# Kernel tuning notes

Hardware: AMD Instinct MI355X
Metric: run time of the kernel (lower is better)

Reference implementation:

```python
import jax, jax.numpy as jnp
import numpy as np

N_ITERS = 3  # Set2Set n_iters


def _set2set(feat, gid, B, Wih, Whh, bih, bhh):
    # DGL Set2Set with n_iters=3, n_layers=1: LSTM(input=2D, hidden=D), PyTorch gate order i,f,g,o
    N, D = feat.shape
    q_star = jnp.zeros((B, 2 * D), feat.dtype)
    h = jnp.zeros((B, D), feat.dtype)
    c = jnp.zeros((B, D), feat.dtype)
    bias = bih + bhh
    for _ in range(N_ITERS):
        gates = q_star @ Wih.T + h @ Whh.T + bias  # (B, 4D)
        i, f, g, o = jnp.split(gates, 4, axis=-1)
        i = jax.nn.sigmoid(i); f = jax.nn.sigmoid(f); o = jax.nn.sigmoid(o); g = jnp.tanh(g)
        c = f * c + i * g
        h = o * jnp.tanh(c)  # q = h, shape (B, D)
        e = jnp.sum(feat * h[gid], axis=-1)  # (N,) attention logits
        m = jax.ops.segment_max(e, gid, num_segments=B, indices_are_sorted=True)
        ex = jnp.exp(e - m[gid])
        s = jax.ops.segment_sum(ex, gid, num_segments=B, indices_are_sorted=True)
        alpha = ex / s[gid]  # segment softmax
        readout = jax.ops.segment_sum(feat * alpha[:, None], gid, num_segments=B, indices_are_sorted=True)
        q_star = jnp.concatenate([h, readout], axis=-1)  # (B, 2D)
    return q_star


def setup_inputs() -> dict:
    key = jax.random.key(0)
    ks = jax.random.split(key, 18)
    N, E, D, B, OUT = 100000, 1000000, 64, 64, 1
    s = 1.0 / np.sqrt(D)
    u = lambda k, shp, b: jax.random.uniform(k, shp, jnp.float32, -b, b)
    inp = {
        'feat': jax.random.normal(ks[0], (N, D), jnp.float32),
        'efeat': jax.random.normal(ks[1], (E, D), jnp.float32),
        'edge_dst': jax.random.randint(ks[2], (E,), 0, N, jnp.int32),
        'node_graph': jnp.sort(jax.random.randint(ks[3], (N,), 0, B, jnp.int32)),
        'n_graphs': B,
        'node_Wih': u(ks[4], (4 * D, 2 * D), s), 'node_Whh': u(ks[5], (4 * D, D), s),
        'node_bih': u(ks[6], (4 * D,), s), 'node_bhh': u(ks[7], (4 * D,), s),
        'edge_Wih': u(ks[8], (4 * D, 2 * D), s), 'edge_Whh': u(ks[9], (4 * D, D), s),
        'edge_bih': u(ks[10], (4 * D,), s), 'edge_bhh': u(ks[11], (4 * D,), s),
        'W1': u(ks[12], (32, 4 * D), np.sqrt(6.0 / (4 * D + 32)) * np.sqrt(2.0)),
        'b1': jnp.zeros((32,), jnp.float32),
        'W2': u(ks[13], (16, 32), np.sqrt(6.0 / 48) * np.sqrt(2.0)),
        'b2': jnp.zeros((16,), jnp.float32),
        'W3': u(ks[14], (OUT, 16), np.sqrt(6.0 / (16 + OUT)) * np.sqrt(2.0)),
        'b3': jnp.zeros((OUT,), jnp.float32),
    }
    return inp


def reference(feat, efeat, edge_dst, node_graph, n_graphs,
              node_Wih, node_Whh, node_bih, node_bhh,
              edge_Wih, edge_Whh, edge_bih, edge_bhh,
              W1, b1, W2, b2, W3, b3):
    N = feat.shape[0]
    # mpnn = identity: node_emb = feat, edge_emb = efeat
    node_s2s = _set2set(feat, node_graph, n_graphs, node_Wih, node_Whh, node_bih, node_bhh)
    # graph.update_all(fn.copy_e, fn.mean): scatter-mean of edge features onto dst nodes
    deg = jax.ops.segment_sum(jnp.ones((efeat.shape[0],), feat.dtype), edge_dst, num_segments=N)
    edge_agg = jax.ops.segment_sum(efeat, edge_dst, num_segments=N) / jnp.maximum(deg, 1.0)[:, None]
    edge_s2s = _set2set(edge_agg, node_graph, n_graphs, edge_Wih, edge_Whh, edge_bih, edge_bhh)
    out = jnp.concatenate([node_s2s, edge_s2s], axis=1)  # (B, 4D)
    out = jax.nn.relu(out @ W1.T + b1)
    out = jax.nn.relu(out @ W2.T + b2)
    out = out @ W3.T + b3
    return out
```

## Files before the change

### kernel.cpp

```cpp
#include <hip/hip_runtime.h>
#include <math.h>

#define D 64
#define B 64
#define NPB 128
#define NSLOT 4
#define SCAN_BS 1024

__device__ __forceinline__ unsigned encf(float x) {
  unsigned u = __float_as_uint(x);
  return (u & 0x80000000u) ? ~u : (u | 0x80000000u);
}
__device__ __forceinline__ float decf(unsigned e) {
  return (e & 0x80000000u) ? __uint_as_float(e ^ 0x80000000u) : __uint_as_float(~e);
}
__device__ __forceinline__ float sigm(float x) { return 1.0f / (1.0f + __expf(-x)); }


__global__ void k_deg(const int* __restrict__ edge_dst, int* __restrict__ deg, int E) {
  int i = blockIdx.x * blockDim.x + threadIdx.x;
  if (i < E) atomicAdd(&deg[edge_dst[i]], 1);
}

__global__ void k_scan1(const int* __restrict__ deg, int* __restrict__ row_start,
                        int* __restrict__ blocksum, int N) {
  __shared__ int sm[SCAN_BS];
  int t = threadIdx.x;
  int base = blockIdx.x * SCAN_BS;
  int v = (base + t < N) ? deg[base + t] : 0;
  sm[t] = v;
  __syncthreads();
  for (int ofs = 1; ofs < SCAN_BS; ofs <<= 1) {
    int add = (t >= ofs) ? sm[t - ofs] : 0;
    __syncthreads();
    sm[t] += add;
    __syncthreads();
  }
  if (base + t < N) row_start[base + t] = sm[t] - v;
  if (t == SCAN_BS - 1) blocksum[blockIdx.x] = sm[t];
}

__global__ void k_scan2(int* __restrict__ blocksum, int nb) {
  __shared__ int sm[128];
  int t = threadIdx.x;
  int v = (t < nb) ? blocksum[t] : 0;
  sm[t] = v;
  __syncthreads();
  for (int ofs = 1; ofs < 128; ofs <<= 1) {
    int add = (t >= ofs) ? sm[t - ofs] : 0;
    __syncthreads();
    sm[t] += add;
    __syncthreads();
  }
  if (t < nb) blocksum[t] = sm[t] - v;
}

__global__ void k_scan3(int* __restrict__ row_start, const int* __restrict__ blocksum,
                        int* __restrict__ cursor, int N) {
  int n = blockIdx.x * blockDim.x + threadIdx.x;
  if (n < N) {
    int v = row_start[n] + blocksum[n / SCAN_BS];
    row_start[n] = v;
    cursor[n] = v;
  }
}

__global__ void k_fill(const int* __restrict__ edge_dst, int* __restrict__ cursor,
                       int* __restrict__ csr, int E) {
  int e = blockIdx.x * blockDim.x + threadIdx.x;
  if (e < E) {
    int dst = edge_dst[e];
    int idx = atomicAdd(&cursor[dst], 1);
    csr[idx] = e;
  }
}

__global__ void k_gather(const float* __restrict__ efeat, const int* __restrict__ csr,
                         const int* __restrict__ row_start, const int* __restrict__ deg,
                         float* __restrict__ edge_agg, int N) {
  int grp = (blockIdx.x * blockDim.x + threadIdx.x) >> 4;
  int l16 = threadIdx.x & 15;
  if (grp >= N) return;
  int base = row_start[grp];
  int dg = deg[grp];
  float4 acc = make_float4(0.f, 0.f, 0.f, 0.f);
  for (int i = 0; i < dg; i += 16) {
    int idx[16];
    #pragma unroll
    for (int j = 0; j < 16; ++j) {
      int k = i + j;
      idx[j] = csr[base + (k < dg ? k : dg - 1)];
    }
    #pragma unroll
    for (int j = 0; j < 16; ++j) {
      float4 v = *(const float4*)(efeat + (size_t)idx[j] * D + l16 * 4);
      bool ok = (i + j < dg);
      acc.x += ok ? v.x : 0.0f;
      acc.y += ok ? v.y : 0.0f;
      acc.z += ok ? v.z : 0.0f;
      acc.w += ok ? v.w : 0.0f;
    }
  }
  float inv = 1.0f / fmaxf((float)dg, 1.0f);
  acc.x *= inv; acc.y *= inv; acc.z *= inv; acc.w *= inv;
  *(float4*)(edge_agg + (size_t)grp * D + l16 * 4) = acc;
}


__global__ void k_lstm2(int first, float* __restrict__ h2, float* __restrict__ c2,
                        float* __restrict__ s2, float* __restrict__ r2,
                        unsigned* __restrict__ m2, float* __restrict__ off2,
                        const float* __restrict__ nWih, const float* __restrict__ nWhh,
                        const float* __restrict__ nbih, const float* __restrict__ nbhh,
                        const float* __restrict__ eWih, const float* __restrict__ eWhh,
                        const float* __restrict__ ebih, const float* __restrict__ ebhh) {
  __shared__ float sq[2 * D], sg[4 * D];
  int side = blockIdx.y;
  const float* Wih = side ? eWih : nWih;
  const float* Whh = side ? eWhh : nWhh;
  const float* bih = side ? ebih : nbih;
  const float* bhh = side ? ebhh : nbhh;
  float* h = h2 + side * B * D;
  float* c = c2 + side * B * D;
  float* s_buf = s2 + side * B;
  float* r_buf = r2 + side * B * D;

  int b = blockIdx.x, j = threadIdx.x;
  if (j < D) {
    sq[j] = h[b * D + j];
  } else if (j < 2 * D) {
    sq[j] = first ? 0.0f : (r_buf[b * D + (j - D)] / s_buf[b]);
  }
  __syncthreads();
  float acc = bih[j] + bhh[j];
  const float* wr = Wih + (size_t)j * (2 * D);
  #pragma unroll 8
  for (int k = 0; k < 2 * D; ++k) acc += sq[k] * wr[k];
  const float* wr2 = Whh + (size_t)j * D;
  #pragma unroll 8
  for (int k = 0; k < D; ++k) acc += sq[k] * wr2[k];
  sg[j] = acc;
  __syncthreads();
  if (j < D) {
    float ig = sigm(sg[j]);
    float fg = sigm(sg[D + j]);
    float gg = tanhf(sg[2 * D + j]);
    float og = sigm(sg[3 * D + j]);
    float cn = fg * c[b * D + j] + ig * gg;
    c[b * D + j] = cn;
    h[b * D + j] = og * tanhf(cn);
    r_buf[b * D + j] = 0.0f;
  }
  if (j == D) s_buf[b] = 0.0f;
  if (j == D + 1) {
    int idx = side * B + b;
    off2[idx] = first ? 0.0f : decf(m2[idx]);
    m2[idx] = 0u;
  }
}

__global__ void k_att_fused(const float* __restrict__ feat, const float* __restrict__ edge_agg,
                            const int* __restrict__ gid, const float* __restrict__ h2,
                            const float* __restrict__ off2, unsigned* __restrict__ m2,
                            float* __restrict__ s2, float* __restrict__ r2, int N) {
  __shared__ float r_lds[16 * NSLOT * D];
  __shared__ float s_lds[16 * NSLOT];
  __shared__ float m_lds[16 * NSLOT];
  __shared__ float h_lds[NSLOT * D];
  __shared__ float o_lds[NSLOT];
  __shared__ int sg_first;
  __shared__ int used[NSLOT];

  int side = blockIdx.y;
  const float* F = side ? edge_agg : feat;
  const float* h = h2 + side * B * D;
  const float* off = off2 + side * B;
  unsigned* m_enc = m2 + side * B;
  float* s_buf = s2 + side * B;
  float* r_buf = r2 + side * B * D;

  int tid = threadIdx.x;
  int grp = tid >> 4;
  int d4  = tid & 15;
  int base = blockIdx.x * NPB;

  for (int i = tid; i < 16 * NSLOT * D; i += 256) r_lds[i] = 0.0f;
  if (tid < 16 * NSLOT) { s_lds[tid] = 0.0f; m_lds[tid] = -3.4e38f; }
  if (tid < NSLOT) used[tid] = 0;
  if (tid == 0) sg_first = gid[base];
  __syncthreads();
  int gfirst = sg_first;
  {
    int slot = tid >> 6, dim = tid & 63;
    int g = gfirst + slot;
    if (g < B) {
      h_lds[tid] = h[g * D + dim];
      if (dim == 0) o_lds[slot] = off[g];
    }
  }
  __syncthreads();

  float4 acc = make_float4(0.f, 0.f, 0.f, 0.f);
  float sum_ex = 0.0f;
  float local_max = -3.4e38f;
  int cur_g = -1;

  for (int it = 0; it < NPB / 32; ++it) {
    int n0 = base + it * 32 + grp;
    int n1 = n0 + 16;
    bool ok0 = n0 < N, ok1 = n1 < N;
    int g0 = ok0 ? gid[n0] : -1;
    int g1 = ok1 ? gid[n1] : -1;
    float4 f0 = make_float4(0,0,0,0), f1 = make_float4(0,0,0,0);
    float dot0 = 0.f, dot1 = 0.f, ex0 = 0.f, ex1 = 0.f;
    if (ok0) {
      f0 = *(const float4*)(F + (size_t)n0 * D + d4 * 4);
      int s0 = g0 - gfirst;
      float4 hv = (s0 >= 0 && s0 < NSLOT) ? *(const float4*)&h_lds[(s0 << 6) + (d4 << 2)]
                                          : *(const float4*)(h + (size_t)g0 * D + d4 * 4);
      dot0 = f0.x * hv.x + f0.y * hv.y + f0.z * hv.z + f0.w * hv.w;
    }
    if (ok1) {
      f1 = *(const float4*)(F + (size_t)n1 * D + d4 * 4);
      int s1 = g1 - gfirst;
      float4 hv = (s1 >= 0 && s1 < NSLOT) ? *(const float4*)&h_lds[(s1 << 6) + (d4 << 2)]
                                          : *(const float4*)(h + (size_t)g1 * D + d4 * 4);
      dot1 = f1.x * hv.x + f1.y * hv.y + f1.z * hv.z + f1.w * hv.w;
    }
    dot0 += __shfl_xor(dot0, 1); dot1 += __shfl_xor(dot1, 1);
    dot0 += __shfl_xor(dot0, 2); dot1 += __shfl_xor(dot1, 2);
    dot0 += __shfl_xor(dot0, 4); dot1 += __shfl_xor(dot1, 4);
    dot0 += __shfl_xor(dot0, 8); dot1 += __shfl_xor(dot1, 8);
    if (ok0) {
      int s0 = g0 - gfirst;
      ex0 = __expf(dot0 - ((s0 >= 0 && s0 < NSLOT) ? o_lds[s0] : off[g0]));
    }
    if (ok1) {
      int s1 = g1 - gfirst;
      ex1 = __expf(dot1 - ((s1 >= 0 && s1 < NSLOT) ? o_lds[s1] : off[g1]));
    }

    #pragma unroll
    for (int pair = 0; pair < 2; ++pair) {
      bool ok = pair ? ok1 : ok0;
      int g = pair ? g1 : g0;
      float ex = pair ? ex1 : ex0;
      float dt = pair ? dot1 : dot0;
      float4 f = pair ? f1 : f0;
      if (!ok) continue;
      if (g != cur_g) {
        if (cur_g >= 0) {
          int slot = cur_g - gfirst;
          if (slot >= 0 && slot < NSLOT) {
            float4* p = (float4*)&r_lds[((grp * NSLOT + slot) << 6) + (d4 << 2)];
            float4 v = *p;
            v.x += acc.x; v.y += acc.y; v.z += acc.z; v.w += acc.w;
            *p = v;
            if (d4 == 0) {
              s_lds[grp * NSLOT + slot] += sum_ex;
              m_lds[grp * NSLOT + slot] = fmaxf(m_lds[grp * NSLOT + slot], local_max);
              used[slot] = 1;
            }
          } else {
            float* rp = r_buf + cur_g * D + d4 * 4;
            atomicAdd(rp + 0, acc.x); atomicAdd(rp + 1, acc.y);
            atomicAdd(rp + 2, acc.z); atomicAdd(rp + 3, acc.w);
            if (d4 == 0) { atomicAdd(&s_buf[cur_g], sum_ex); atomicMax(&m_enc[cur_g], encf(local_max)); }
          }
        }
        cur_g = g; acc = make_float4(0,0,0,0); sum_ex = 0.f; local_max = -3.4e38f;
      }
      acc.x += ex * f.x; acc.y += ex * f.y; acc.z += ex * f.z; acc.w += ex * f.w;
      if (d4 == 0) { sum_ex += ex; local_max = fmaxf(local_max, dt); }
    }
  }
  if (cur_g >= 0) {
    int slot = cur_g - gfirst;
    if (slot >= 0 && slot < NSLOT) {
      float4* p = (float4*)&r_lds[((grp * NSLOT + slot) << 6) + (d4 << 2)];
      float4 v = *p;
      v.x += acc.x; v.y += acc.y; v.z += acc.z; v.w += acc.w;
      *p = v;
      if (d4 == 0) {
        s_lds[grp * NSLOT + slot] += sum_ex;
        m_lds[grp * NSLOT + slot] = fmaxf(m_lds[grp * NSLOT + slot], local_max);
        used[slot] = 1;
      }
    } else {
      float* rp = r_buf + cur_g * D + d4 * 4;
      atomicAdd(rp + 0, acc.x); atomicAdd(rp + 1, acc.y);
      atomicAdd(rp + 2, acc.z); atomicAdd(rp + 3, acc.w);
      if (d4 == 0) { atomicAdd(&s_buf[cur_g], sum_ex); atomicMax(&m_enc[cur_g], encf(local_max)); }
    }
  }
  __syncthreads();

  {
    int slot = tid >> 6, dim = tid & 63;
    int g = gfirst + slot;
    if (g < B && used[slot]) {
      float sum = 0.0f;
      #pragma unroll
      for (int q = 0; q < 16; ++q) sum += r_lds[((q * NSLOT + slot) << 6) + dim];
      atomicAdd(&r_buf[g * D + dim], sum);
    }
  }
  if (tid < NSLOT) {
    int g = gfirst + tid;
    if (g < B && used[tid]) {
      float ssum = 0.0f;
      #pragma unroll
      for (int q = 0; q < 16; ++q) ssum += s_lds[q * NSLOT + tid];
      atomicAdd(&s_buf[g], ssum);
    }
  } else if (tid >= 64 && tid < 64 + NSLOT) {
    int slot = tid - 64;
    int g = gfirst + slot;
    if (g < B && used[slot]) {
      float mmax = -3.4e38f;
      #pragma unroll
      for (int q = 0; q < 16; ++q) mmax = fmaxf(mmax, m_lds[q * NSLOT + slot]);
      atomicMax(&m_enc[g], encf(mmax));
    }
  }
}

__global__ void k_mlp(const float* __restrict__ h2, const float* __restrict__ r2,
                      const float* __restrict__ s2,
                      const float* __restrict__ W1, const float* __restrict__ b1,
                      const float* __restrict__ W2, const float* __restrict__ b2,
                      const float* __restrict__ W3, const float* __restrict__ b3,
                      float* __restrict__ out) {
  __shared__ float x[4 * D], h1[32], h2s[16];
  int b = blockIdx.x, t = threadIdx.x;
  x[t]       = (t < D) ? h2[b * D + t]         : r2[b * D + (t - D)] / s2[b];
  x[128 + t] = (t < D) ? h2[B * D + b * D + t] : r2[B * D + b * D + (t - D)] / s2[B + b];
  __syncthreads();
  if (t < 32) {
    float acc = b1[t];
    const float* w = W1 + (size_t)t * (4 * D);
    #pragma unroll 8
    for (int k = 0; k < 4 * D; ++k) acc += x[k] * w[k];
    h1[t] = fmaxf(acc, 0.0f);
  }
  __syncthreads();
  if (t < 16) {
    float acc = b2[t];
    const float* w = W2 + (size_t)t * 32;
    #pragma unroll
    for (int k = 0; k < 32; ++k) acc += h1[k] * w[k];
    h2s[t] = fmaxf(acc, 0.0f);
  }
  __syncthreads();
  if (t == 0) {
    float acc = b3[0];
    #pragma unroll
    for (int k = 0; k < 16; ++k) acc += h2s[k] * W3[k];
    out[b] = acc;
  }
}


extern "C" void kernel_launch(void* const* d_in, const int* in_sizes, int n_in,
                              void* d_out, int out_size, void* d_ws, size_t ws_size,
                              hipStream_t stream) {
  const float* feat      = (const float*)d_in[0];
  const float* efeat     = (const float*)d_in[1];
  const int*   edge_dst  = (const int*)d_in[2];
  const int*   node_graph= (const int*)d_in[3];
  const float* node_Wih  = (const float*)d_in[5];
  const float* node_Whh  = (const float*)d_in[6];
  const float* node_bih  = (const float*)d_in[7];
  const float* node_bhh  = (const float*)d_in[8];
  const float* edge_Wih  = (const float*)d_in[9];
  const float* edge_Whh  = (const float*)d_in[10];
  const float* edge_bih  = (const float*)d_in[11];
  const float* edge_bhh  = (const float*)d_in[12];
  const float* W1 = (const float*)d_in[13];
  const float* b1 = (const float*)d_in[14];
  const float* W2 = (const float*)d_in[15];
  const float* b2 = (const float*)d_in[16];
  const float* W3 = (const float*)d_in[17];
  const float* b3 = (const float*)d_in[18];
  float* out = (float*)d_out;

  const int N = in_sizes[0] / D;
  const int E = in_sizes[2];

  float* ws = (float*)d_ws;
  size_t off = 0;
  float* edge_agg = ws + off; off += (size_t)N * D;
  float* h2       = ws + off; off += 2 * B * D;
  float* c2       = ws + off; off += 2 * B * D;
  float* s2       = ws + off; off += 2 * B;
  float* r2       = ws + off; off += 2 * B * D;
  float* off2     = ws + off; off += 2 * B;
  unsigned* m2    = (unsigned*)(ws + off); off += 2 * B;
  int* deg        = (int*)(ws + off); off += N;
  int* row_start  = (int*)(ws + off); off += N;
  int* cursor     = (int*)(ws + off); off += N;
  int* blocksum   = (int*)(ws + off); off += 128;
  int* csr        = (int*)(ws + off); off += E + 8;

  hipMemsetAsync(deg, 0, (size_t)N * sizeof(int), stream);
  hipMemsetAsync(h2, 0, (size_t)(4 * B * D) * sizeof(float), stream);

  const int nb = (N + SCAN_BS - 1) / SCAN_BS;
  k_deg<<<(E + 255) / 256, 256, 0, stream>>>(edge_dst, deg, E);
  k_scan1<<<nb, SCAN_BS, 0, stream>>>(deg, row_start, blocksum, N);
  k_scan2<<<1, 128, 0, stream>>>(blocksum, nb);
  k_scan3<<<(N + 255) / 256, 256, 0, stream>>>(row_start, blocksum, cursor, N);
  k_fill<<<(E + 255) / 256, 256, 0, stream>>>(edge_dst, cursor, csr, E);

  k_gather<<<(N + 15) / 16, 256, 0, stream>>>(efeat, csr, row_start, deg, edge_agg, N);

  const int att_blocks = (N + NPB - 1) / NPB;
  dim3 ga(att_blocks, 2), gb(B, 2);

  for (int it = 0; it < 3; ++it) {
    k_lstm2<<<gb, 256, 0, stream>>>(it == 0 ? 1 : 0, h2, c2, s2, r2, m2, off2,
                                    node_Wih, node_Whh, node_bih, node_bhh,
                                    edge_Wih, edge_Whh, edge_bih, edge_bhh);
    k_att_fused<<<ga, 256, 0, stream>>>(feat, edge_agg, node_graph, h2, off2, m2, s2, r2, N);
  }

  k_mlp<<<B, 128, 0, stream>>>(h2, r2, s2, W1, b1, W2, b2, W3, b3, out);
}
```

Baseline: 261.1 us.

## Fuse degree count with first LSTM step and merge scan kernels

Merges the degree-count kernel with the first LSTM iteration into one launch, since the first LSTM step does not depend on the graph data. Folds the block-sum scan into the scan-apply kernel, so each block redundantly rescans the 98 block sums instead of launching a separate kernel. Combines the two memsets into one by reordering the workspace, and stages the node graph ids in LDS in the attention kernel. The aim is fewer launches and less serialization, at the cost of redundant per-block scan work and a more tangled kernel.

Result: no change. 261.0 us (-0.1%).

```diff
diff --git a/kernel.cpp b/kernel.cpp
--- a/kernel.cpp
+++ b/kernel.cpp
@@ -17,9 +17,77 @@
 __device__ __forceinline__ float sigm(float x) { return 1.0f / (1.0f + __expf(-x)); }
 
 
-__global__ void k_deg(const int* __restrict__ edge_dst, int* __restrict__ deg, int E) {
-  int i = blockIdx.x * blockDim.x + threadIdx.x;
-  if (i < E) atomicAdd(&deg[edge_dst[i]], 1);
+__device__ __forceinline__ void lstm_body(int side, int b, int first,
+    float* __restrict__ h2, float* __restrict__ c2,
+    float* __restrict__ s2, float* __restrict__ r2,
+    unsigned* __restrict__ m2, float* __restrict__ off2,
+    const float* __restrict__ nWih, const float* __restrict__ nWhh,
+    const float* __restrict__ nbih, const float* __restrict__ nbhh,
+    const float* __restrict__ eWih, const float* __restrict__ eWhh,
+    const float* __restrict__ ebih, const float* __restrict__ ebhh,
+    float* sq, float* sg) {
+  const float* Wih = side ? eWih : nWih;
+  const float* Whh = side ? eWhh : nWhh;
+  const float* bih = side ? ebih : nbih;
+  const float* bhh = side ? ebhh : nbhh;
+  float* h = h2 + side * B * D;
+  float* c = c2 + side * B * D;
+  float* s_buf = s2 + side * B;
+  float* r_buf = r2 + side * B * D;
+
+  int j = threadIdx.x;
+  if (j < D) {
+    sq[j] = h[b * D + j];
+  } else if (j < 2 * D) {
+    sq[j] = first ? 0.0f : (r_buf[b * D + (j - D)] / s_buf[b]);
+  }
+  __syncthreads();
+  float acc = bih[j] + bhh[j];
+  const float* wr = Wih + (size_t)j * (2 * D);
+  #pragma unroll 8
+  for (int k = 0; k < 2 * D; ++k) acc += sq[k] * wr[k];
+  const float* wr2 = Whh + (size_t)j * D;
+  #pragma unroll 8
+  for (int k = 0; k < D; ++k) acc += sq[k] * wr2[k];
+  sg[j] = acc;
+  __syncthreads();
+  if (j < D) {
+    float ig = sigm(sg[j]);
+    float fg = sigm(sg[D + j]);
+    float gg = tanhf(sg[2 * D + j]);
+    float og = sigm(sg[3 * D + j]);
+    float cn = fg * c[b * D + j] + ig * gg;
+    c[b * D + j] = cn;
+    h[b * D + j] = og * tanhf(cn);
+    r_buf[b * D + j] = 0.0f;
+  }
+  if (j == D) s_buf[b] = 0.0f;
+  if (j == D + 1) {
+    int idx = side * B + b;
+    off2[idx] = first ? 0.0f : decf(m2[idx]);
+    m2[idx] = 0u;
+  }
+}
+
+
+__global__ void k_deg_lstm(int DEG, const int* __restrict__ edge_dst, int* __restrict__ deg, int E,
+                           float* __restrict__ h2, float* __restrict__ c2,
+                           float* __restrict__ s2, float* __restrict__ r2,
+                           unsigned* __restrict__ m2, float* __restrict__ off2,
+                           const float* __restrict__ nWih, const float* __restrict__ nWhh,
+                           const float* __restrict__ nbih, const float* __restrict__ nbhh,
+                           const float* __restrict__ eWih, const float* __restrict__ eWhh,
+                           const float* __restrict__ ebih, const float* __restrict__ ebhh) {
+  __shared__ float sq[2 * D], sg[4 * D];
+  int bx = blockIdx.x;
+  if (bx < DEG) {
+    int i = bx * 256 + threadIdx.x;
+    if (i < E) atomicAdd(&deg[edge_dst[i]], 1);
+  } else {
+    int j = bx - DEG;
+    lstm_body(j >> 6, j & 63, 1, h2, c2, s2, r2, m2, off2,
+              nWih, nWhh, nbih, nbhh, eWih, eWhh, ebih, ebhh, sq, sg);
+  }
 }
 
 __global__ void k_scan1(const int* __restrict__ deg, int* __restrict__ row_start,
@@ -40,26 +108,22 @@
   if (t == SCAN_BS - 1) blocksum[blockIdx.x] = sm[t];
 }
 
-__global__ void k_scan2(int* __restrict__ blocksum, int nb) {
+__global__ void k_scan3(int* __restrict__ row_start, const int* __restrict__ blocksum,
+                        int* __restrict__ cursor, int N, int nb) {
   __shared__ int sm[128];
   int t = threadIdx.x;
-  int v = (t < nb) ? blocksum[t] : 0;
-  sm[t] = v;
+  if (t < 128) sm[t] = (t < nb) ? blocksum[t] : 0;
   __syncthreads();
   for (int ofs = 1; ofs < 128; ofs <<= 1) {
-    int add = (t >= ofs) ? sm[t - ofs] : 0;
+    int add = (t < 128 && t >= ofs) ? sm[t - ofs] : 0;
     __syncthreads();
-    sm[t] += add;
+    if (t < 128) sm[t] += add;
     __syncthreads();
   }
-  if (t < nb) blocksum[t] = sm[t] - v;
-}
-
-__global__ void k_scan3(int* __restrict__ row_start, const int* __restrict__ blocksum,
-                        int* __restrict__ cursor, int N) {
-  int n = blockIdx.x * blockDim.x + threadIdx.x;
+  int n = blockIdx.x * 256 + t;
   if (n < N) {
-    int v = row_start[n] + blocksum[n / SCAN_BS];
+    int c = n / SCAN_BS;
+    int v = row_start[n] + ((c > 0) ? sm[c - 1] : 0);
     row_start[n] = v;
     cursor[n] = v;
   }
@@ -74,6 +138,7 @@
     csr[idx] = e;
   }
 }
+
 
 __global__ void k_gather(const float* __restrict__ efeat, const int* __restrict__ csr,
                          const int* __restrict__ row_start, const int* __restrict__ deg,
@@ -115,49 +180,10 @@
                         const float* __restrict__ eWih, const float* __restrict__ eWhh,
                         const float* __restrict__ ebih, const float* __restrict__ ebhh) {
   __shared__ float sq[2 * D], sg[4 * D];
-  int side = blockIdx.y;
-  const float* Wih = side ? eWih : nWih;
-  const float* Whh = side ? eWhh : nWhh;
-  const float* bih = side ? ebih : nbih;
-  const float* bhh = side ? ebhh : nbhh;
-  float* h = h2 + side * B * D;
-  float* c = c2 + side * B * D;
-  float* s_buf = s2 + side * B;
-  float* r_buf = r2 + side * B * D;
-
-  int b = blockIdx.x, j = threadIdx.x;
-  if (j < D) {
-    sq[j] = h[b * D + j];
-  } else if (j < 2 * D) {
-    sq[j] = first ? 0.0f : (r_buf[b * D + (j - D)] / s_buf[b]);
-  }
-  __syncthreads();
-  float acc = bih[j] + bhh[j];
-  const float* wr = Wih + (size_t)j * (2 * D);
-  #pragma unroll 8
-  for (int k = 0; k < 2 * D; ++k) acc += sq[k] * wr[k];
-  const float* wr2 = Whh + (size_t)j * D;
-  #pragma unroll 8
-  for (int k = 0; k < D; ++k) acc += sq[k] * wr2[k];
-  sg[j] = acc;
-  __syncthreads();
-  if (j < D) {
-    float ig = sigm(sg[j]);
-    float fg = sigm(sg[D + j]);
-    float gg = tanhf(sg[2 * D + j]);
-    float og = sigm(sg[3 * D + j]);
-    float cn = fg * c[b * D + j] + ig * gg;
-    c[b * D + j] = cn;
-    h[b * D + j] = og * tanhf(cn);
-    r_buf[b * D + j] = 0.0f;
-  }
-  if (j == D) s_buf[b] = 0.0f;
-  if (j == D + 1) {
-    int idx = side * B + b;
-    off2[idx] = first ? 0.0f : decf(m2[idx]);
-    m2[idx] = 0u;
-  }
-}
+  lstm_body(blockIdx.y, blockIdx.x, first, h2, c2, s2, r2, m2, off2,
+            nWih, nWhh, nbih, nbhh, eWih, eWhh, ebih, ebhh, sq, sg);
+}
+
 
 __global__ void k_att_fused(const float* __restrict__ feat, const float* __restrict__ edge_agg,
                             const int* __restrict__ gid, const float* __restrict__ h2,
@@ -168,7 +194,7 @@
   __shared__ float m_lds[16 * NSLOT];
   __shared__ float h_lds[NSLOT * D];
   __shared__ float o_lds[NSLOT];
-  __shared__ int sg_first;
+  __shared__ int gid_lds[NPB];
   __shared__ int used[NSLOT];
 
   int side = blockIdx.y;
@@ -187,9 +213,9 @@
   for (int i = tid; i < 16 * NSLOT * D; i += 256) r_lds[i] = 0.0f;
   if (tid < 16 * NSLOT) { s_lds[tid] = 0.0f; m_lds[tid] = -3.4e38f; }
   if (tid < NSLOT) used[tid] = 0;
-  if (tid == 0) sg_first = gid[base];
-  __syncthreads();
-  int gfirst = sg_first;
+  if (tid < NPB) gid_lds[tid] = gid[min(base + tid, N - 1)];
+  __syncthreads();
+  const int gfirst = gid_lds[0];
   {
     int slot = tid >> 6, dim = tid & 63;
     int g = gfirst + slot;
@@ -206,11 +232,12 @@
   int cur_g = -1;
 
   for (int it = 0; it < NPB / 32; ++it) {
-    int n0 = base + it * 32 + grp;
+    int p0 = it * 32 + grp;
+    int n0 = base + p0;
     int n1 = n0 + 16;
     bool ok0 = n0 < N, ok1 = n1 < N;
-    int g0 = ok0 ? gid[n0] : -1;
-    int g1 = ok1 ? gid[n1] : -1;
+    int g0 = gid_lds[p0];
+    int g1 = gid_lds[p0 + 16];
     float4 f0 = make_float4(0,0,0,0), f1 = make_float4(0,0,0,0);
     float dot0 = 0.f, dot1 = 0.f, ex0 = 0.f, ex1 = 0.f;
     if (ok0) {
@@ -325,6 +352,7 @@
   }
 }
 
+
 __global__ void k_mlp(const float* __restrict__ h2, const float* __restrict__ r2,
                       const float* __restrict__ s2,
                       const float* __restrict__ W1, const float* __restrict__ b1,
@@ -389,36 +417,37 @@
 
   float* ws = (float*)d_ws;
   size_t off = 0;
-  float* edge_agg = ws + off; off += (size_t)N * D;
+  int* deg        = (int*)(ws + off); off += N;
   float* h2       = ws + off; off += 2 * B * D;
   float* c2       = ws + off; off += 2 * B * D;
+  float* edge_agg = ws + off; off += (size_t)N * D;
   float* s2       = ws + off; off += 2 * B;
   float* r2       = ws + off; off += 2 * B * D;
   float* off2     = ws + off; off += 2 * B;
   unsigned* m2    = (unsigned*)(ws + off); off += 2 * B;
-  int* deg        = (int*)(ws + off); off += N;
   int* row_start  = (int*)(ws + off); off += N;
   int* cursor     = (int*)(ws + off); off += N;
   int* blocksum   = (int*)(ws + off); off += 128;
   int* csr        = (int*)(ws + off); off += E + 8;
 
-  hipMemsetAsync(deg, 0, (size_t)N * sizeof(int), stream);
-  hipMemsetAsync(h2, 0, (size_t)(4 * B * D) * sizeof(float), stream);
-
-  const int nb = (N + SCAN_BS - 1) / SCAN_BS;
-  k_deg<<<(E + 255) / 256, 256, 0, stream>>>(edge_dst, deg, E);
+  hipMemsetAsync(ws, 0, ((size_t)N + 4 * B * D) * sizeof(float), stream);
+
+  const int nb  = (N + SCAN_BS - 1) / SCAN_BS;
+  const int DEG = (E + 255) / 256;
+  const int ATT = (N + NPB - 1) / NPB;
+
+  k_deg_lstm<<<DEG + 128, 256, 0, stream>>>(DEG, edge_dst, deg, E, h2, c2, s2, r2, m2, off2,
+      node_Wih, node_Whh, node_bih, node_bhh, edge_Wih, edge_Whh, edge_bih, edge_bhh);
   k_scan1<<<nb, SCAN_BS, 0, stream>>>(deg, row_start, blocksum, N);
-  k_scan2<<<1, 128, 0, stream>>>(blocksum, nb);
-  k_scan3<<<(N + 255) / 256, 256, 0, stream>>>(row_start, blocksum, cursor, N);
-  k_fill<<<(E + 255) / 256, 256, 0, stream>>>(edge_dst, cursor, csr, E);
+  k_scan3<<<(N + 255) / 256, 256, 0, stream>>>(row_start, blocksum, cursor, N, nb);
+  k_fill<<<DEG, 256, 0, stream>>>(edge_dst, cursor, csr, E);
 
   k_gather<<<(N + 15) / 16, 256, 0, stream>>>(efeat, csr, row_start, deg, edge_agg, N);
 
-  const int att_blocks = (N + NPB - 1) / NPB;
-  dim3 ga(att_blocks, 2), gb(B, 2);
-
-  for (int it = 0; it < 3; ++it) {
-    k_lstm2<<<gb, 256, 0, stream>>>(it == 0 ? 1 : 0, h2, c2, s2, r2, m2, off2,
+  dim3 ga(ATT, 2), gb(B, 2);
+  k_att_fused<<<ga, 256, 0, stream>>>(feat, edge_agg, node_graph, h2, off2, m2, s2, r2, N);
+  for (int it = 1; it < 3; ++it) {
+    k_lstm2<<<gb, 256, 0, stream>>>(0, h2, c2, s2, r2, m2, off2,
                                     node_Wih, node_Whh, node_bih, node_bhh,
                                     edge_Wih, edge_Whh, edge_bih, edge_bhh);
     k_att_fused<<<ga, 256, 0, stream>>>(feat, edge_agg, node_graph, h2, off2, m2, s2, r2, N);
```
